# Performance work log

Measured on AMD Instinct MI355X. Metric: run time of the kernel, lower is better.

Reference implementation:

```python
import jax, jax.numpy as jnp
import numpy as np

TAU = 0.2
EPS = 1e-12  # matches torch F.normalize eps


def setup_inputs() -> dict:
    key = jax.random.key(0)
    k1, k2 = jax.random.split(key)
    N, D = 8192, 128
    h1 = jax.random.normal(k1, (N, D), dtype=jnp.float32)
    h2 = jax.random.normal(k2, (N, D), dtype=jnp.float32)
    return {"h1": h1, "h2": h2}


def _l2norm(x):
    # torch.nn.functional.normalize: x / max(||x||, eps)
    n = jnp.sqrt(jnp.sum(x * x, axis=1, keepdims=True))
    return x / jnp.maximum(n, EPS)


def _nt_xent(h1, h2):
    h1n = _l2norm(h1)
    h2n = _l2norm(h2)
    inter = jnp.exp((h1n @ h1n.T) / TAU)  # [N, N]
    intra = jnp.exp((h1n @ h2n.T) / TAU)  # [N, N]
    pos = jnp.diagonal(intra)
    neg = inter.sum(axis=1) + intra.sum(axis=1) - jnp.diagonal(inter)
    return -jnp.log(pos / neg)  # [N]


def reference(h1, h2):
    l1 = _nt_xent(h1, h2)
    l2 = _nt_xent(h2, h1)
    return jnp.mean((l1 + l2) * 0.5)
```

## Files before the change

### kernel.cpp

```cpp
#include <hip/hip_runtime.h>
#include <math.h>


constexpr int D = 128;
constexpr float E5 = 148.4131591025766f;
constexpr int NSLOT = 145;

typedef __attribute__((ext_vector_type(16))) float f32x16;
typedef __attribute__((ext_vector_type(8)))  int   v8i;
typedef __attribute__((ext_vector_type(4)))  long  v4l;

__global__ __launch_bounds__(256) void normalize_kernel(
    const float4* __restrict__ h1, const float4* __restrict__ h2,
    unsigned char* __restrict__ P, float* __restrict__ d12,
    float* __restrict__ out, int N)
{
    const float SC = sqrtf(5.0f * 1.44269504088896340736f);
    if (blockIdx.x == 0 && threadIdx.x == 0) out[0] = 0.f;

    const int tx   = threadIdx.x;
    const int rloc = tx >> 3;
    const int t    = tx & 7;
    const int row  = blockIdx.x * 32 + rloc;

    float4 u[4], w[4];
#pragma unroll
    for (int i = 0; i < 4; ++i) {
        u[i] = h1[(size_t)row * 32 + t * 4 + i];
        w[i] = h2[(size_t)row * 32 + t * 4 + i];
    }
    float ss1 = 0.f, ss2 = 0.f, s12 = 0.f;
#pragma unroll
    for (int i = 0; i < 4; ++i) {
        ss1 += u[i].x*u[i].x + u[i].y*u[i].y + u[i].z*u[i].z + u[i].w*u[i].w;
        ss2 += w[i].x*w[i].x + w[i].y*w[i].y + w[i].z*w[i].z + w[i].w*w[i].w;
        s12 += u[i].x*w[i].x + u[i].y*w[i].y + u[i].z*w[i].z + u[i].w*w[i].w;
    }
#pragma unroll
    for (int off = 4; off > 0; off >>= 1) {
        ss1 += __shfl_xor(ss1, off, 64);
        ss2 += __shfl_xor(ss2, off, 64);
        s12 += __shfl_xor(s12, off, 64);
    }
    float n1 = fmaxf(sqrtf(ss1), 1e-12f);
    float n2 = fmaxf(sqrtf(ss2), 1e-12f);
    float c1 = SC / n1, c2 = SC / n2;
    if (t == 0) d12[row] = 5.f * s12 / (n1 * n2);

    int u0 = __builtin_amdgcn_cvt_pk_fp8_f32(u[0].x*c1, u[0].y*c1, 0, false);
    u0     = __builtin_amdgcn_cvt_pk_fp8_f32(u[0].z*c1, u[0].w*c1, u0, true);
    int u1 = __builtin_amdgcn_cvt_pk_fp8_f32(u[1].x*c1, u[1].y*c1, 0, false);
    u1     = __builtin_amdgcn_cvt_pk_fp8_f32(u[1].z*c1, u[1].w*c1, u1, true);
    int u2 = __builtin_amdgcn_cvt_pk_fp8_f32(u[2].x*c1, u[2].y*c1, 0, false);
    u2     = __builtin_amdgcn_cvt_pk_fp8_f32(u[2].z*c1, u[2].w*c1, u2, true);
    int u3 = __builtin_amdgcn_cvt_pk_fp8_f32(u[3].x*c1, u[3].y*c1, 0, false);
    u3     = __builtin_amdgcn_cvt_pk_fp8_f32(u[3].z*c1, u[3].w*c1, u3, true);
    int w0 = __builtin_amdgcn_cvt_pk_fp8_f32(w[0].x*c2, w[0].y*c2, 0, false);
    w0     = __builtin_amdgcn_cvt_pk_fp8_f32(w[0].z*c2, w[0].w*c2, w0, true);
    int w1 = __builtin_amdgcn_cvt_pk_fp8_f32(w[1].x*c2, w[1].y*c2, 0, false);
    w1     = __builtin_amdgcn_cvt_pk_fp8_f32(w[1].z*c2, w[1].w*c2, w1, true);
    int w2 = __builtin_amdgcn_cvt_pk_fp8_f32(w[2].x*c2, w[2].y*c2, 0, false);
    w2     = __builtin_amdgcn_cvt_pk_fp8_f32(w[2].z*c2, w[2].w*c2, w2, true);
    int w3 = __builtin_amdgcn_cvt_pk_fp8_f32(w[3].x*c2, w[3].y*c2, 0, false);
    w3     = __builtin_amdgcn_cvt_pk_fp8_f32(w[3].z*c2, w[3].w*c2, w3, true);

    unsigned long long ulo = (unsigned)u0 | ((unsigned long long)(unsigned)u1 << 32);
    unsigned long long uhi = (unsigned)u2 | ((unsigned long long)(unsigned)u3 << 32);
    unsigned long long wlo = (unsigned)w0 | ((unsigned long long)(unsigned)w1 << 32);
    unsigned long long whi = (unsigned)w2 | ((unsigned long long)(unsigned)w3 << 32);

    size_t b1 = (size_t)blockIdx.x * 4096 + (size_t)t * 512 + (size_t)rloc * 8;
    size_t b2 = ((size_t)(N >> 5) + blockIdx.x) * 4096 + (size_t)t * 512 + (size_t)rloc * 8;
    *(unsigned long long*)(P + b1)       = ulo;
    *(unsigned long long*)(P + b1 + 256) = uhi;
    *(unsigned long long*)(P + b2)       = wlo;
    *(unsigned long long*)(P + b2 + 256) = whi;
}

__device__ __forceinline__ v8i load_op(const unsigned char* p) {
    v4l t;
    t[0] = *(const long*)(p);
    t[1] = *(const long*)(p + 256);
    t[2] = *(const long*)(p + 512);
    t[3] = *(const long*)(p + 768);
    return __builtin_bit_cast(v8i, t);
}

__global__ __launch_bounds__(256, 3) void gram_mfma_kernel(
    const unsigned char* __restrict__ P, float* __restrict__ part, int N)
{
    const int I = blockIdx.x;
    const int z = blockIdx.z;
    int nT = 4, dBase = 0;
    bool doCols = true;
    if (blockIdx.y < 16) { dBase = blockIdx.y * 4; }
    else                 { nT = 1; dBase = 64; doCols = false; }

    __shared__ float ldsRow[64];
    __shared__ float ldsCol[4][128];

    const int tx   = threadIdx.x;
    const int lane = tx & 63;
    const int l32  = lane & 31, lhi = lane >> 5;
    const int wid  = tx >> 6;
    const int wr   = wid >> 1;
    const int wc   = wid & 1;
    const int iBase = I * 128 + z * 64;
    const int fOff = lhi * 1024;

    if (tx < 64) ldsRow[tx] = 0.f;
    ((float*)ldsCol)[tx] = 0.f;
    ((float*)ldsCol)[tx + 256] = 0.f;
    __syncthreads();

    v8i a[2];
    {
        const unsigned char* xp =
            P + (size_t)(I * 4 + z * 2 + wr) * 4096 + fOff + l32 * 8;
        a[0] = load_op(xp);
        a[1] = load_op(xp + 2048);
    }

    float racc[16];
#pragma unroll
    for (int r = 0; r < 16; ++r) racc[r] = 0.f;

    const int j0 = wc * 64 + l32;

    v8i b0[2], b1[2];
    {
        const int J0 = (I + dBase) & 127;
        const unsigned char* pb =
            P + (size_t)(J0 * 4 + wc * 2) * 4096 + fOff + l32 * 8;
#pragma unroll
        for (int kc = 0; kc < 2; ++kc) {
            b0[kc] = load_op(pb + kc * 2048);
            b1[kc] = load_op(pb + 4096 + kc * 2048);
        }
    }

#pragma unroll
    for (int t = 0; t < 4; ++t) {
        if (t >= nT) break;

        const int tn = (t + 1 < nT) ? t + 1 : t;
        const int Jn = (I + dBase + tn) & 127;
        const unsigned char* pn =
            P + (size_t)(Jn * 4 + wc * 2) * 4096 + fOff + l32 * 8;
        v8i n0[2], n1[2];
#pragma unroll
        for (int kc = 0; kc < 2; ++kc) {
            n0[kc] = load_op(pn + kc * 2048);
            n1[kc] = load_op(pn + 4096 + kc * 2048);
        }

        f32x16 acc0, acc1;
#pragma unroll
        for (int r = 0; r < 16; ++r) { acc0[r] = 0.f; acc1[r] = 0.f; }

#pragma unroll
        for (int kc = 0; kc < 2; ++kc) {
            acc0 = __builtin_amdgcn_mfma_scale_f32_32x32x64_f8f6f4(
                a[kc], b0[kc], acc0, 0, 0, 0, 127, 0, 127);
            acc1 = __builtin_amdgcn_mfma_scale_f32_32x32x64_f8f6f4(
                a[kc], b1[kc], acc1, 0, 0, 0, 127, 0, 127);
        }

        float c0 = 0.f, c1 = 0.f;
#pragma unroll
        for (int r = 0; r < 16; ++r) {
            float e0 = __builtin_amdgcn_exp2f(acc0[r]);
            float e1 = __builtin_amdgcn_exp2f(acc1[r]);
            racc[r] += e0 + e1;
            c0 += e0;
            c1 += e1;
        }
        if (doCols && (dBase + t) != 0) {
            c0 += __shfl_xor(c0, 32, 64);
            c1 += __shfl_xor(c1, 32, 64);
            if (lane < 32) {
                atomicAdd(&ldsCol[t][j0], c0);
                atomicAdd(&ldsCol[t][j0 + 32], c1);
            }
        }

        b0[0] = n0[0]; b0[1] = n0[1];
        b1[0] = n1[0]; b1[1] = n1[1];
    }

#pragma unroll
    for (int r = 0; r < 16; ++r) {
        float s = racc[r];
#pragma unroll
        for (int off = 1; off < 32; off <<= 1)
            s += __shfl_xor(s, off, 64);
        if (l32 == 0) {
            int rowm = (r & 3) + 8 * (r >> 2) + 4 * lhi;
            atomicAdd(&ldsRow[wr * 32 + rowm], s);
        }
    }

    __syncthreads();

    {
        const int y = blockIdx.y;
        if (tx < 64)
            part[(size_t)y * (2 * N) + iBase + tx] = ldsRow[tx];
        if (doCols && tx < 128) {
#pragma unroll
            for (int t = 0; t < 4; ++t) {
                const int J = (I + dBase + t) & 127;
                const size_t slot = (size_t)(17 + (y * 4 + t) * 2 + z);
                part[slot * (2 * N) + (size_t)J * 128 + tx] = ldsCol[t][tx];
            }
        }
    }
}

__global__ __launch_bounds__(256) void loss_reduce_kernel(
    const float* __restrict__ part, const float* __restrict__ d12,
    float* __restrict__ out, int N)
{
    __shared__ float sm[256];
    float s = 0.f;
    for (int i = blockIdx.x * 256 + threadIdx.x; i < N; i += gridDim.x * 256) {
        float r1 = 0.f, r2 = 0.f;
#pragma unroll 5
        for (int sl = 0; sl < NSLOT; ++sl) {
            r1 += part[(size_t)sl * (2 * N) + i];
            r2 += part[(size_t)sl * (2 * N) + N + i];
        }
        s += 0.5f * (logf(r1 - E5) + logf(r2 - E5)) - d12[i];
    }
    sm[threadIdx.x] = s;
    __syncthreads();
    for (int w = 128; w > 0; w >>= 1) {
        if (threadIdx.x < w) sm[threadIdx.x] += sm[threadIdx.x + w];
        __syncthreads();
    }
    if (threadIdx.x == 0) atomicAdd(out, sm[0] / (float)N);
}

extern "C" void kernel_launch(void* const* d_in, const int* in_sizes, int n_in,
                              void* d_out, int out_size, void* d_ws, size_t ws_size,
                              hipStream_t stream) {
    const float* h1 = (const float*)d_in[0];
    const float* h2 = (const float*)d_in[1];
    const int N = in_sizes[0] / D;

    unsigned char* P = (unsigned char*)d_ws;
    float* part = (float*)(P + (size_t)2 * N * D);
    float* d12  = part + (size_t)NSLOT * 2 * N;
    float* out  = (float*)d_out;

    normalize_kernel<<<N / 32, 256, 0, stream>>>(
        (const float4*)h1, (const float4*)h2, P, d12, out, N);

    dim3 grid(128, 17, 2);
    gram_mfma_kernel<<<grid, 256, 0, stream>>>(P, part, N);

    loss_reduce_kernel<<<64, 256, 0, stream>>>(part, d12, out, N);
}
```

Baseline: 132.4 us.

## Pack FP8 operands contiguously, widen occupancy, and parallelize slot reduction

The packed FP8 operand buffer is re-laid out so each lane's MFMA operand occupies 32 contiguous bytes. The normalize kernel can then store 16-byte vectors, and the gram kernel can load with two 16-byte loads instead of four strided 8-byte loads. The gram kernel's launch bound goes from 3 to 4 blocks per SM, which tightens the register budget. The loss reduction now gives 8 warps per block to the 145 partial slots of 32 rows and launches N/32 blocks instead of 64, so far more threads share the memory-bound slot sum; in exchange it issues more atomics.

```diff
diff --git a/kernel.cpp b/kernel.cpp
--- a/kernel.cpp
+++ b/kernel.cpp
@@ -9,6 +9,7 @@
 typedef __attribute__((ext_vector_type(16))) float f32x16;
 typedef __attribute__((ext_vector_type(8)))  int   v8i;
 typedef __attribute__((ext_vector_type(4)))  long  v4l;
+typedef __attribute__((ext_vector_type(2)))  long  v2l;
 
 __global__ __launch_bounds__(256) void normalize_kernel(
     const float4* __restrict__ h1, const float4* __restrict__ h2,
@@ -69,24 +70,22 @@
     unsigned long long wlo = (unsigned)w0 | ((unsigned long long)(unsigned)w1 << 32);
     unsigned long long whi = (unsigned)w2 | ((unsigned long long)(unsigned)w3 << 32);
 
-    size_t b1 = (size_t)blockIdx.x * 4096 + (size_t)t * 512 + (size_t)rloc * 8;
-    size_t b2 = ((size_t)(N >> 5) + blockIdx.x) * 4096 + (size_t)t * 512 + (size_t)rloc * 8;
-    *(unsigned long long*)(P + b1)       = ulo;
-    *(unsigned long long*)(P + b1 + 256) = uhi;
-    *(unsigned long long*)(P + b2)       = wlo;
-    *(unsigned long long*)(P + b2 + 256) = whi;
+    const size_t opoff = (size_t)((t >> 2) * 2 + ((t >> 1) & 1)) * 1024
+                       + (size_t)rloc * 32 + (size_t)((2 * t) & 3) * 8;
+    size_t b1 = (size_t)blockIdx.x * 4096 + opoff;
+    size_t b2 = ((size_t)(N >> 5) + blockIdx.x) * 4096 + opoff;
+    *(v2l*)(P + b1) = (v2l){(long)ulo, (long)uhi};
+    *(v2l*)(P + b2) = (v2l){(long)wlo, (long)whi};
 }
 
 __device__ __forceinline__ v8i load_op(const unsigned char* p) {
-    v4l t;
-    t[0] = *(const long*)(p);
-    t[1] = *(const long*)(p + 256);
-    t[2] = *(const long*)(p + 512);
-    t[3] = *(const long*)(p + 768);
+    v2l q0 = *(const v2l*)(p);
+    v2l q1 = *(const v2l*)(p + 16);
+    v4l t = {q0[0], q0[1], q1[0], q1[1]};
     return __builtin_bit_cast(v8i, t);
 }
 
-__global__ __launch_bounds__(256, 3) void gram_mfma_kernel(
+__global__ __launch_bounds__(256, 4) void gram_mfma_kernel(
     const unsigned char* __restrict__ P, float* __restrict__ part, int N)
 {
     const int I = blockIdx.x;
@@ -106,7 +105,7 @@
     const int wr   = wid >> 1;
     const int wc   = wid & 1;
     const int iBase = I * 128 + z * 64;
-    const int fOff = lhi * 1024;
+    const int fOff = lhi * 1024 + l32 * 32;
 
     if (tx < 64) ldsRow[tx] = 0.f;
     ((float*)ldsCol)[tx] = 0.f;
@@ -116,7 +115,7 @@
     v8i a[2];
     {
         const unsigned char* xp =
-            P + (size_t)(I * 4 + z * 2 + wr) * 4096 + fOff + l32 * 8;
+            P + (size_t)(I * 4 + z * 2 + wr) * 4096 + fOff;
         a[0] = load_op(xp);
         a[1] = load_op(xp + 2048);
     }
@@ -131,7 +130,7 @@
     {
         const int J0 = (I + dBase) & 127;
         const unsigned char* pb =
-            P + (size_t)(J0 * 4 + wc * 2) * 4096 + fOff + l32 * 8;
+            P + (size_t)(J0 * 4 + wc * 2) * 4096 + fOff;
 #pragma unroll
         for (int kc = 0; kc < 2; ++kc) {
             b0[kc] = load_op(pb + kc * 2048);
@@ -146,7 +145,7 @@
         const int tn = (t + 1 < nT) ? t + 1 : t;
         const int Jn = (I + dBase + tn) & 127;
         const unsigned char* pn =
-            P + (size_t)(Jn * 4 + wc * 2) * 4096 + fOff + l32 * 8;
+            P + (size_t)(Jn * 4 + wc * 2) * 4096 + fOff;
         v8i n0[2], n1[2];
 #pragma unroll
         for (int kc = 0; kc < 2; ++kc) {
@@ -221,24 +220,31 @@
     const float* __restrict__ part, const float* __restrict__ d12,
     float* __restrict__ out, int N)
 {
-    __shared__ float sm[256];
-    float s = 0.f;
-    for (int i = blockIdx.x * 256 + threadIdx.x; i < N; i += gridDim.x * 256) {
-        float r1 = 0.f, r2 = 0.f;
-#pragma unroll 5
-        for (int sl = 0; sl < NSLOT; ++sl) {
-            r1 += part[(size_t)sl * (2 * N) + i];
-            r2 += part[(size_t)sl * (2 * N) + N + i];
-        }
-        s += 0.5f * (logf(r1 - E5) + logf(r2 - E5)) - d12[i];
-    }
-    sm[threadIdx.x] = s;
+    __shared__ float lr1[8][32];
+    __shared__ float lr2[8][32];
+    const int j = threadIdx.x & 31;
+    const int s = threadIdx.x >> 5;
+    const int i = blockIdx.x * 32 + j;
+
+    float r1 = 0.f, r2 = 0.f;
+    for (int sl = s; sl < NSLOT; sl += 8) {
+        r1 += part[(size_t)sl * (2 * N) + i];
+        r2 += part[(size_t)sl * (2 * N) + N + i];
+    }
+    lr1[s][j] = r1;
+    lr2[s][j] = r2;
     __syncthreads();
-    for (int w = 128; w > 0; w >>= 1) {
-        if (threadIdx.x < w) sm[threadIdx.x] += sm[threadIdx.x + w];
-        __syncthreads();
-    }
-    if (threadIdx.x == 0) atomicAdd(out, sm[0] / (float)N);
+
+    if (threadIdx.x < 32) {
+        float a1 = 0.f, a2 = 0.f;
+#pragma unroll
+        for (int ss = 0; ss < 8; ++ss) { a1 += lr1[ss][j]; a2 += lr2[ss][j]; }
+        float loss = 0.5f * (logf(a1 - E5) + logf(a2 - E5)) - d12[i];
+#pragma unroll
+        for (int off = 1; off < 32; off <<= 1)
+            loss += __shfl_xor(loss, off, 64);
+        if (j == 0) atomicAdd(out, loss / (float)N);
+    }
 }
 
 extern "C" void kernel_launch(void* const* d_in, const int* in_sizes, int n_in,
@@ -259,5 +265,5 @@
     dim3 grid(128, 17, 2);
     gram_mfma_kernel<<<grid, 256, 0, stream>>>(P, part, N);
 
-    loss_reduce_kernel<<<64, 256, 0, stream>>>(part, d12, out, N);
-}
+    loss_reduce_kernel<<<N / 32, 256, 0, stream>>>(part, d12, out, N);
+}
```

Result: slower. 147.9 us (+11.7%).
